# Performance work log

Hardware: AMD Instinct MI355X
Metric: run time of the kernel (lower is better)

Reference implementation:

```python
import jax, jax.numpy as jnp
import numpy as np

H_DIM = 2048
N_HEADS = 16

def setup_inputs() -> dict:
    key = jax.random.key(0)
    ks = jax.random.split(key, 9)
    B, T, C = 2, 2048, H_DIM
    scale = 1.0 / np.sqrt(C)  # lecun_normal approx
    src = jax.random.normal(ks[0], (B, T, C), dtype=jnp.float32)
    Wq = jax.random.normal(ks[1], (C, H_DIM), dtype=jnp.float32) * scale
    Wk = jax.random.normal(ks[2], (C, H_DIM), dtype=jnp.float32) * scale
    Wv = jax.random.normal(ks[3], (C, H_DIM), dtype=jnp.float32) * scale
    Wo = jax.random.normal(ks[4], (H_DIM, H_DIM), dtype=jnp.float32) * scale
    bq = jnp.zeros((H_DIM,), jnp.float32)
    bk = jnp.zeros((H_DIM,), jnp.float32)
    bv = jnp.zeros((H_DIM,), jnp.float32)
    bo = jnp.zeros((H_DIM,), jnp.float32)
    return {"src": src, "Wq": Wq, "bq": bq, "Wk": Wk, "bk": bk,
            "Wv": Wv, "bv": bv, "Wo": Wo, "bo": bo}

def reference(src, Wq, bq, Wk, bk, Wv, bv, Wo, bo):
    B, T, C = src.shape
    N = N_HEADS
    D = C // N
    def heads(x):  # [B,T,h_dim] -> [B,N,T,D]
        return x.reshape(B, T, N, D).transpose(0, 2, 1, 3)
    q = heads(src @ Wq + bq)
    k = heads(src @ Wk + bk)
    v = heads(src @ Wv + bv)
    # scaled dot-product with causal mask
    scores = jnp.einsum('bntd,bnsd->bnts', q, k) / jnp.sqrt(jnp.float32(D))
    causal = jnp.tril(jnp.ones((T, T), dtype=bool))
    scores = jnp.where(causal[None, None], scores, -jnp.inf)
    attn = jax.nn.softmax(scores, axis=-1)
    out = jnp.einsum('bnts,bnsd->bntd', attn, v)  # dropout is identity (drop_p=0)
    out = out.transpose(0, 2, 1, 3).reshape(B, T, N * D)
    return out @ Wo + bo
```

## Files before the change

### kernel.cpp

```cpp
#include <hip/hip_runtime.h>
#include <hip/hip_bf16.h>

typedef float f32x4 __attribute__((ext_vector_type(4)));
typedef __bf16 bf16x8v __attribute__((ext_vector_type(8)));
typedef __bf16 bf16x4v __attribute__((ext_vector_type(4)));
typedef unsigned uint2v __attribute__((ext_vector_type(2)));
typedef bf16x8v __attribute__((may_alias)) bf16x8;
typedef bf16x4v __attribute__((may_alias)) bf16x4;
typedef uint2v __attribute__((may_alias)) u32x2;

typedef __attribute__((address_space(1))) const void gvoid_t;
typedef __attribute__((address_space(3))) void lvoid_t;

#define DEVINL __device__ __forceinline__

#define BDIM 2
#define TDIM 2048
#define CDIM 2048
#define NHEAD 16
#define DHEAD 128
#define MROWS 4096
#define WSZ ((size_t)CDIM * CDIM)
#define XSZ ((size_t)MROWS * CDIM)

#define BARRIER_LGKM() asm volatile("s_waitcnt lgkmcnt(0)\ns_barrier" ::: "memory")

DEVINL __bf16 f2bf(float f) {
  unsigned u = __builtin_bit_cast(unsigned, f);
  u += 0x7fffu + ((u >> 16) & 1u);
  unsigned short h = (unsigned short)(u >> 16);
  return __builtin_bit_cast(__bf16, h);
}

DEVINL unsigned pk2bf_trunc(float lo, float hi) {
  return __builtin_amdgcn_perm(__builtin_bit_cast(unsigned, hi),
                               __builtin_bit_cast(unsigned, lo), 0x07060302);
}

DEVINL void gl2lds16(const void* g, void* l) {
  __builtin_amdgcn_global_load_lds((gvoid_t*)g, (lvoid_t*)l, 16, 0, 0);
}

__global__ void detect_dtype(const unsigned* __restrict__ w,
                             int* __restrict__ flag, int* __restrict__ cnt) {
  const int l = threadIdx.x;
  if (l == 0) *cnt = 0;
  const unsigned word = w[l];
  const unsigned e = (word >> 7) & 0xFFu;
  const int vote = (e >= 0x70u && e <= 0x87u) ? 1 : 0;
  const unsigned long long m = __ballot(vote);
  if (l == 0) *flag = (__popcll(m) >= 32) ? 1 : 0;
}

__global__ __launch_bounds__(256) void cvt_src(const void* __restrict__ in,
                                               __bf16* __restrict__ out,
                                               const int* __restrict__ flag,
                                               int n8) {
  const int i = blockIdx.x * 256 + threadIdx.x;
  if (i >= n8) return;
  if (*flag) {
    ((bf16x8*)out)[i] = ((const bf16x8*)in)[i];
  } else {
    const float* f = (const float*)in + (size_t)i * 8;
    bf16x8v v;
#pragma unroll
    for (int j = 0; j < 8; ++j) v[j] = f2bf(f[j]);
    ((bf16x8*)out)[i] = v;
  }
}

__global__ __launch_bounds__(256) void cvt_wt(
    const void* __restrict__ w0, const void* __restrict__ w1,
    const void* __restrict__ w2, const void* __restrict__ w3,
    __bf16* __restrict__ out, const int* __restrict__ flag) {
  __shared__ __attribute__((aligned(16))) __bf16 tile[64][68];
  const void* W = (blockIdx.z == 0) ? w0 : (blockIdx.z == 1) ? w1
                : (blockIdx.z == 2) ? w2 : w3;
  __bf16* Wt = out + (size_t)blockIdx.z * WSZ;
  const int tx = threadIdx.x & 63, ty = threadIdx.x >> 6;
  const int k0 = blockIdx.x * 64, n0 = blockIdx.y * 64;
  const int fl = *flag;
#pragma unroll
  for (int i = ty; i < 64; i += 4) {
    const size_t off = (size_t)(k0 + i) * CDIM + n0 + tx;
    const float v = fl ? (float)((const __bf16*)W)[off] : ((const float*)W)[off];
    tile[i][tx] = f2bf(v);
  }
  __syncthreads();
#pragma unroll
  for (int i = ty; i < 64; i += 4)
    Wt[(size_t)(n0 + i) * CDIM + k0 + tx] = tile[tx][i];
}

__global__ __launch_bounds__(256) void cvt_bias(
    const void* __restrict__ b0, const void* __restrict__ b1,
    const void* __restrict__ b2, const void* __restrict__ b3,
    float* __restrict__ out, const int* __restrict__ flag) {
  const int i = blockIdx.x * 256 + threadIdx.x;
  const void* b = (i < 2048) ? b0 : (i < 4096) ? b1 : (i < 6144) ? b2 : b3;
  const int idx = i & 2047;
  out[i] = (*flag) ? (float)((const __bf16*)b)[idx] : ((const float*)b)[idx];
}

template <int MODE>
__global__ __launch_bounds__(512, 2) void gemmring(
    const __bf16* __restrict__ A, const __bf16* __restrict__ Bt,
    const float* __restrict__ bias, __bf16* __restrict__ qb,
    __bf16* __restrict__ kb, __bf16* __restrict__ vtb,
    const int* __restrict__ flag, void* __restrict__ outp) {
  constexpr int K = CDIM;
  constexpr int NKT = K / 64;
  __shared__ __attribute__((aligned(16))) __bf16 Asl[4][128 * 32];
  __shared__ __attribute__((aligned(16))) __bf16 Bsl[4][256 * 32];

  const int tid = threadIdx.x;
  const int w = tid >> 6, l = tid & 63;
  const int quad = l >> 4, l16 = l & 15;
  const int wm = w >> 2, wn = w & 3;

  const int bid = blockIdx.x;
  const int bm = bid & 31, bn = bid >> 5;
  const int m0 = bm * 128, n0 = bn * 256;

  const int ls = (tid & 7) ^ ((tid >> 3) & 7);
  const int rbase = 2 * (tid >> 3) + (ls >> 2);
  const int cb8 = (ls & 3) * 8;
  const __bf16* gAh = A + (size_t)(m0 + rbase) * K + cb8;
  const __bf16* gBh = Bt + (size_t)(n0 + rbase) * K + cb8;

  const int L2 = l16 >> 1;
  const int physr = (((l16 & 1) << 2) + quad) ^ L2;
  const int lane_e = L2 * 64 + physr * 8;

#define STAGE_A(h)                                                       \
  gl2lds16(gAh + (size_t)(((h) >> 1) * 64 + ((h) & 1) * 32),             \
           (__bf16*)Asl[(h) & 3] + w * 512)
#define STAGE_B(h, e)                                                    \
  gl2lds16(gBh + (size_t)(e) * 128 * K +                                 \
               (((h) >> 1) * 64 + ((h) & 1) * 32),                       \
           (__bf16*)Bsl[(h) & 3] + (e) * 4096 + w * 512)

  f32x4 acc[4][4];
#pragma unroll
  for (int i = 0; i < 4; ++i)
#pragma unroll
    for (int j = 0; j < 4; ++j) acc[i][j] = (f32x4){0.f, 0.f, 0.f, 0.f};

  STAGE_A(0); STAGE_B(0, 0); STAGE_B(0, 1);
  STAGE_A(1); STAGE_B(1, 0); STAGE_B(1, 1);
  STAGE_A(2); STAGE_B(2, 0); STAGE_B(2, 1);
  asm volatile("s_waitcnt vmcnt(6)" ::: "memory");
  __builtin_amdgcn_sched_barrier(0);
  __builtin_amdgcn_s_barrier();

#define MFMA8(NF0)                                                        \
  __builtin_amdgcn_s_setprio(1);                                          \
  _Pragma("unroll") for (int mi = 0; mi < 4; ++mi) {                      \
    acc[mi][(NF0)] = __builtin_amdgcn_mfma_f32_16x16x32_bf16(             \
        afr[mi], bfr[0], acc[mi][(NF0)], 0, 0, 0);                        \
    acc[mi][(NF0) + 1] = __builtin_amdgcn_mfma_f32_16x16x32_bf16(         \
        afr[mi], bfr[1], acc[mi][(NF0) + 1], 0, 0, 0);                    \
  }                                                                       \
  __builtin_amdgcn_s_setprio(0);

#define LGKM_BAR()                                                        \
  __builtin_amdgcn_s_barrier();                                           \
  asm volatile("s_waitcnt lgkmcnt(0)" ::: "memory");                      \
  __builtin_amdgcn_sched_barrier(0)

  for (int kt = 0; kt < NKT; ++kt) {
    const int h0 = 2 * kt;
    const __bf16* Ab0 = Asl[h0 & 3];
    const __bf16* Bb0 = Bsl[h0 & 3];
    const __bf16* Ab1 = Asl[(h0 + 1) & 3];
    const __bf16* Bb1 = Bsl[(h0 + 1) & 3];
    bf16x8 afr[4], bfr[2];

#pragma unroll
    for (int mi = 0; mi < 4; ++mi)
      afr[mi] = *(const bf16x8*)&Ab0[(wm * 64 + mi * 16) * 32 + lane_e];
    bfr[0] = *(const bf16x8*)&Bb0[(wn * 64 + 0 * 16) * 32 + lane_e];
    bfr[1] = *(const bf16x8*)&Bb0[(wn * 64 + 1 * 16) * 32 + lane_e];
    if (kt <= NKT - 2) { STAGE_A(h0 + 3); STAGE_B(h0 + 3, 0); }
    LGKM_BAR();
    MFMA8(0)
    __builtin_amdgcn_s_barrier();

    bfr[0] = *(const bf16x8*)&Bb0[(wn * 64 + 2 * 16) * 32 + lane_e];
    bfr[1] = *(const bf16x8*)&Bb0[(wn * 64 + 3 * 16) * 32 + lane_e];
    if (kt <= NKT - 2) { STAGE_B(h0 + 3, 1); }
    LGKM_BAR();
    MFMA8(2)
    if (kt < NKT - 1)
      asm volatile("s_waitcnt vmcnt(6)" ::: "memory");
    else
      asm volatile("s_waitcnt vmcnt(0)" ::: "memory");
    __builtin_amdgcn_sched_barrier(0);
    __builtin_amdgcn_s_barrier();

#pragma unroll
    for (int mi = 0; mi < 4; ++mi)
      afr[mi] = *(const bf16x8*)&Ab1[(wm * 64 + mi * 16) * 32 + lane_e];
    bfr[0] = *(const bf16x8*)&Bb1[(wn * 64 + 0 * 16) * 32 + lane_e];
    bfr[1] = *(const bf16x8*)&Bb1[(wn * 64 + 1 * 16) * 32 + lane_e];
    if (kt <= NKT - 3) { STAGE_A(h0 + 4); STAGE_B(h0 + 4, 0); }
    LGKM_BAR();
    MFMA8(0)
    __builtin_amdgcn_s_barrier();

    bfr[0] = *(const bf16x8*)&Bb1[(wn * 64 + 2 * 16) * 32 + lane_e];
    bfr[1] = *(const bf16x8*)&Bb1[(wn * 64 + 3 * 16) * 32 + lane_e];
    if (kt <= NKT - 3) { STAGE_B(h0 + 4, 1); }
    LGKM_BAR();
    MFMA8(2)
    if (kt < NKT - 2)
      asm volatile("s_waitcnt vmcnt(6)" ::: "memory");
    else if (kt == NKT - 2)
      asm volatile("s_waitcnt vmcnt(3)" ::: "memory");
    __builtin_amdgcn_sched_barrier(0);
    __builtin_amdgcn_s_barrier();
  }
#undef MFMA8
#undef LGKM_BAR
#undef STAGE_A
#undef STAGE_B

  if (MODE == 0) {
    const int mat = n0 >> 11;
#pragma unroll
    for (int nf = 0; nf < 4; ++nf) {
      const int n = n0 + wn * 64 + nf * 16 + l16;
      const int nn = n & 2047;
      const int h = nn >> 7, d = nn & 127;
      const float bv = bias[n];
#pragma unroll
      for (int mi = 0; mi < 4; ++mi) {
        const int mbase = m0 + wm * 64 + mi * 16 + quad * 4;
        const int bb = mbase >> 11, t = mbase & 2047;
        if (mat == 2) {
          bf16x4v v4;
#pragma unroll
          for (int r = 0; r < 4; ++r) v4[r] = f2bf(acc[mi][nf][r] + bv);
          *(bf16x4*)&vtb[((size_t)(bb * NHEAD + h) * DHEAD + d) * TDIM + t] = v4;
        } else {
          __bf16* op = (mat == 0) ? qb : kb;
#pragma unroll
          for (int r = 0; r < 4; ++r)
            op[((size_t)(bb * NHEAD + h) * TDIM + t + r) * DHEAD + d] =
                f2bf(acc[mi][nf][r] + bv);
        }
      }
    }
  } else {
    const int ofl = *flag;
#pragma unroll
    for (int nf = 0; nf < 4; ++nf) {
      const int n = n0 + wn * 64 + nf * 16 + l16;
      const float bv = bias[n];
#pragma unroll
      for (int mi = 0; mi < 4; ++mi) {
#pragma unroll
        for (int r = 0; r < 4; ++r) {
          const int m = m0 + wm * 64 + mi * 16 + quad * 4 + r;
          const float v = acc[mi][nf][r] + bv;
          if (ofl) ((__bf16*)outp)[(size_t)m * CDIM + n] = f2bf(v);
          else     ((float*)outp)[(size_t)m * CDIM + n] = v;
        }
      }
    }
  }
}

__global__ __launch_bounds__(256, 2) void attn(
    const __bf16* __restrict__ Q, const __bf16* __restrict__ K,
    const __bf16* __restrict__ Vt, __bf16* __restrict__ ctx,
    int* __restrict__ cnt) {
  constexpr float CSC = 0.12753139726f;
  __shared__ __attribute__((aligned(16))) __bf16 Kls[64 * 128];
  __shared__ __attribute__((aligned(16))) __bf16 Vls[128 * 64];
  __shared__ __attribute__((aligned(16))) __bf16 Pls[4][32 * 64];
  __shared__ int jobLds;

  const int tid = threadIdx.x;
  const int w = tid >> 6, l = tid & 63, quad = l >> 4, l16 = l & 15;

  const int krow = tid >> 4;
  const int kcol = tid & 15;
  const int kldsoff = ((kcol ^ krow) * 8);
  const int vrow = tid >> 3;
  const int vcol = tid & 7;
  const int vldsoff = ((vcol ^ (vrow & 7)) * 8);

  for (;;) {
    __syncthreads();
    if (tid == 0) jobLds = atomicAdd(cnt, 1);
    __syncthreads();
    const int j = jobLds;
    if (j >= 512) break;
    const int qt = 15 - (j >> 5);
    const int bh = j & 31;
    const int t0w = qt * 128 + w * 32;
    const __bf16* Qbh = Q + (size_t)bh * TDIM * DHEAD;
    const __bf16* Kbh = K + (size_t)bh * TDIM * DHEAD;
    const __bf16* Vbh = Vt + (size_t)bh * TDIM * DHEAD;

    bf16x8 qf[2][4];
#pragma unroll
    for (int tt = 0; tt < 2; ++tt)
#pragma unroll
      for (int ks = 0; ks < 4; ++ks)
        qf[tt][ks] = *(const bf16x8*)(Qbh +
                     (size_t)(t0w + tt * 16 + l16) * DHEAD + ks * 32 + quad * 8);

    f32x4 oacc[8][2];
#pragma unroll
    for (int dt = 0; dt < 8; ++dt)
#pragma unroll
      for (int tt = 0; tt < 2; ++tt) oacc[dt][tt] = (f32x4){0.f, 0.f, 0.f, 0.f};
    float mrow[2] = {-1e30f, -1e30f};
    float lrow[2] = {0.f, 0.f};

    const int nsb = 2 * (qt + 1);

    bf16x8 kr[4], vr[4];
#pragma unroll
    for (int p = 0; p < 4; ++p)
      kr[p] = *(const bf16x8*)(Kbh + (size_t)(p * 16 + krow) * DHEAD + kcol * 8);
#pragma unroll
    for (int p = 0; p < 4; ++p)
      vr[p] = *(const bf16x8*)(Vbh + (size_t)(p * 32 + vrow) * TDIM + vcol * 8);

    for (int sb = 0; sb < nsb; ++sb) {
      const int s0 = sb * 64;
      BARRIER_LGKM();
#pragma unroll
      for (int p = 0; p < 4; ++p)
        *(bf16x8*)&Kls[(p * 16 + krow) * 128 + kldsoff] = kr[p];
#pragma unroll
      for (int p = 0; p < 4; ++p)
        *(bf16x8*)&Vls[(p * 32 + vrow) * 64 + vldsoff] = vr[p];
      if (sb + 1 < nsb) {
        const int s1 = s0 + 64;
#pragma unroll
        for (int p = 0; p < 4; ++p)
          kr[p] = *(const bf16x8*)(Kbh + (size_t)(s1 + p * 16 + krow) * DHEAD +
                                   kcol * 8);
#pragma unroll
        for (int p = 0; p < 4; ++p)
          vr[p] = *(const bf16x8*)(Vbh + (size_t)(p * 32 + vrow) * TDIM + s1 +
                                   vcol * 8);
      }
      BARRIER_LGKM();
      if (s0 > t0w + 31) continue;

      f32x4 sacc[4][2];
#pragma unroll
      for (int st = 0; st < 4; ++st)
#pragma unroll
        for (int tt = 0; tt < 2; ++tt) sacc[st][tt] = (f32x4){0.f, 0.f, 0.f, 0.f};
#pragma unroll
      for (int ks = 0; ks < 4; ++ks) {
        bf16x8 kf[4];
#pragma unroll
        for (int st = 0; st < 4; ++st)
          kf[st] = *(const bf16x8*)&Kls[(st * 16 + l16) * 128 +
                                        (((ks * 4 + quad) ^ l16) * 8)];
#pragma unroll
        for (int st = 0; st < 4; ++st)
#pragma unroll
          for (int tt = 0; tt < 2; ++tt)
            sacc[st][tt] = __builtin_amdgcn_mfma_f32_16x16x32_bf16(
                kf[st], qf[tt][ks], sacc[st][tt], 0, 0, 0);
      }
      if (s0 + 63 > t0w) {
#pragma unroll
        for (int st = 0; st < 4; ++st)
#pragma unroll
          for (int tt = 0; tt < 2; ++tt)
#pragma unroll
            for (int r = 0; r < 4; ++r) {
              const int s = s0 + st * 16 + quad * 4 + r;
              const int t = t0w + tt * 16 + l16;
              if (s > t) sacc[st][tt][r] = -1e30f;
            }
      }
#pragma unroll
      for (int tt = 0; tt < 2; ++tt) {
        float vm = -1e30f;
#pragma unroll
        for (int st = 0; st < 4; ++st)
#pragma unroll
          for (int r = 0; r < 4; ++r) vm = fmaxf(vm, sacc[st][tt][r]);
        vm = fmaxf(vm, __shfl_xor(vm, 16));
        vm = fmaxf(vm, __shfl_xor(vm, 32));
        const float mnew = fmaxf(mrow[tt], vm);
        if (__ballot(mnew > mrow[tt])) {
          const float alpha = exp2f((mrow[tt] - mnew) * CSC);
          lrow[tt] *= alpha;
#pragma unroll
          for (int dt = 0; dt < 8; ++dt)
#pragma unroll
            for (int r = 0; r < 4; ++r) oacc[dt][tt][r] *= alpha;
          mrow[tt] = mnew;
        }
        float rs = 0.f;
#pragma unroll
        for (int st = 0; st < 4; ++st) {
          const float p0 = exp2f((sacc[st][tt][0] - mnew) * CSC);
          const float p1 = exp2f((sacc[st][tt][1] - mnew) * CSC);
          const float p2 = exp2f((sacc[st][tt][2] - mnew) * CSC);
          const float p3 = exp2f((sacc[st][tt][3] - mnew) * CSC);
          rs += (p0 + p1) + (p2 + p3);
          u32x2 pk = {pk2bf_trunc(p0, p1), pk2bf_trunc(p2, p3)};
          *(u32x2*)&Pls[w][(tt * 16 + l16) * 64 +
                           (((st * 2 + (quad >> 1)) ^ (l16 & 7)) * 8) +
                           (quad & 1) * 4] = pk;
        }
        rs += __shfl_xor(rs, 16);
        rs += __shfl_xor(rs, 32);
        lrow[tt] += rs;
      }
      asm volatile("s_waitcnt lgkmcnt(0)" ::: "memory");
#pragma unroll
      for (int ks = 0; ks < 2; ++ks) {
        bf16x8 pf[2];
#pragma unroll
        for (int tt = 0; tt < 2; ++tt)
          pf[tt] = *(const bf16x8*)&Pls[w][(tt * 16 + l16) * 64 +
                                           (((ks * 4 + quad) ^ (l16 & 7)) * 8)];
#pragma unroll
        for (int dt = 0; dt < 8; ++dt) {
          const bf16x8 vf =
              *(const bf16x8*)&Vls[(dt * 16 + l16) * 64 +
                                   (((ks * 4 + quad) ^ (l16 & 7)) * 8)];
#pragma unroll
          for (int tt = 0; tt < 2; ++tt)
            oacc[dt][tt] = __builtin_amdgcn_mfma_f32_16x16x32_bf16(
                vf, pf[tt], oacc[dt][tt], 0, 0, 0);
        }
      }
    }

    const int b = bh >> 4, h = bh & 15;
#pragma unroll
    for (int tt = 0; tt < 2; ++tt) {
      const float rinv = 1.0f / lrow[tt];
      const int t = t0w + tt * 16 + l16;
      __bf16* cp = ctx + ((size_t)(b * TDIM + t)) * CDIM + h * DHEAD;
#pragma unroll
      for (int dt = 0; dt < 8; ++dt) {
        bf16x4v v4;
#pragma unroll
        for (int r = 0; r < 4; ++r) v4[r] = f2bf(oacc[dt][tt][r] * rinv);
        *(bf16x4*)&cp[dt * 16 + quad * 4] = v4;
      }
    }
  }
}

extern "C" void kernel_launch(void* const* d_in, const int* in_sizes, int n_in,
                              void* d_out, int out_size, void* d_ws,
                              size_t ws_size, hipStream_t stream) {
  const void* src = d_in[0];
  const void* Wq = d_in[1];
  const void* bq = d_in[2];
  const void* Wk = d_in[3];
  const void* bk = d_in[4];
  const void* Wv = d_in[5];
  const void* bv = d_in[6];
  const void* Wo = d_in[7];
  const void* bo = d_in[8];

  char* wsb = (char*)d_ws;
  int* flag = (int*)wsb;
  int* cnt = (int*)(wsb + 128);
  __bf16* srcbf = (__bf16*)(wsb + 256);
  __bf16* wqt = srcbf + XSZ;
  __bf16* wkt = wqt + WSZ;
  __bf16* wvt = wkt + WSZ;
  __bf16* wot = wvt + WSZ;
  __bf16* qb = wot + WSZ;
  __bf16* kb = qb + XSZ;
  __bf16* vtb = kb + XSZ;
  float* biasf = (float*)(vtb + XSZ);
  __bf16* ctx = srcbf;

  detect_dtype<<<1, 64, 0, stream>>>((const unsigned*)src, flag, cnt);
  cvt_src<<<4096, 256, 0, stream>>>(src, srcbf, flag, (int)(XSZ / 8));
  cvt_wt<<<dim3(32, 32, 4), 256, 0, stream>>>(Wq, Wk, Wv, Wo, wqt, flag);
  cvt_bias<<<32, 256, 0, stream>>>(bq, bk, bv, bo, biasf, flag);
  gemmring<0><<<768, 512, 0, stream>>>(srcbf, wqt, biasf, qb, kb, vtb,
                                       nullptr, nullptr);
  attn<<<512, 256, 0, stream>>>(qb, kb, vtb, ctx, cnt);
  gemmring<1><<<256, 512, 0, stream>>>(ctx, wot, biasf + 6144, nullptr,
                                       nullptr, nullptr, flag, d_out);
}
```

Before: 426.6 us.

## Enlarge GEMM block tiles to 256x256 for QKV and 256x128 for output projection

Rewrites the bf16 GEMM kernel to use 256-row block tiles: the QKV projection uses 256x256 tiles with 128x64 warp tiles, and the output projection uses 256x128 tiles with 64x64 warp tiles. Each warp loads four A fragments and four B fragments and reuses them across 16 MFMAs, which raises arithmetic intensity per LDS read. The prefetch pipeline changes from a three-half-stage lookahead to a two-stage-ahead scheme with new vmcnt thresholds. In exchange, the QKV launch has only 384 blocks, LDS use is larger, and register pressure is higher, which may limit occupancy and leave the 256 CUs unevenly loaded.

```diff
diff --git a/kernel.cpp b/kernel.cpp
--- a/kernel.cpp
+++ b/kernel.cpp
@@ -103,127 +103,161 @@
 }
 
 template <int MODE>
-__global__ __launch_bounds__(512, 2) void gemmring(
+__global__ __launch_bounds__(512, 2) void gemm8p(
     const __bf16* __restrict__ A, const __bf16* __restrict__ Bt,
     const float* __restrict__ bias, __bf16* __restrict__ qb,
     __bf16* __restrict__ kb, __bf16* __restrict__ vtb,
     const int* __restrict__ flag, void* __restrict__ outp) {
   constexpr int K = CDIM;
   constexpr int NKT = K / 64;
-  __shared__ __attribute__((aligned(16))) __bf16 Asl[4][128 * 32];
-  __shared__ __attribute__((aligned(16))) __bf16 Bsl[4][256 * 32];
+  constexpr int BN = (MODE == 0) ? 256 : 128;
+  constexpr int WMR = (MODE == 0) ? 128 : 64;
+  constexpr int MF = WMR / 16;
+  constexpr int BLD = BN / 128;
+  __shared__ __attribute__((aligned(16))) __bf16 Asl[4][256 * 32];
+  __shared__ __attribute__((aligned(16))) __bf16 Bsl[4][BN * 32];
 
   const int tid = threadIdx.x;
   const int w = tid >> 6, l = tid & 63;
   const int quad = l >> 4, l16 = l & 15;
-  const int wm = w >> 2, wn = w & 3;
+  const int wm = (MODE == 0) ? (w >> 2) : (w >> 1);
+  const int wn = (MODE == 0) ? (w & 3) : (w & 1);
 
   const int bid = blockIdx.x;
-  const int bm = bid & 31, bn = bid >> 5;
-  const int m0 = bm * 128, n0 = bn * 256;
+  const int bm = bid & 15, bn = bid >> 4;
+  const int m0 = bm * 256, n0 = bn * BN;
 
   const int ls = (tid & 7) ^ ((tid >> 3) & 7);
   const int rbase = 2 * (tid >> 3) + (ls >> 2);
-  const int cb8 = (ls & 3) * 8;
-  const __bf16* gAh = A + (size_t)(m0 + rbase) * K + cb8;
-  const __bf16* gBh = Bt + (size_t)(n0 + rbase) * K + cb8;
+  const int cb8e = (ls & 3) * 8;
+  const __bf16* gA = A + (size_t)(m0 + rbase) * K + cb8e;
+  const __bf16* gB = Bt + (size_t)(n0 + rbase) * K + cb8e;
 
   const int L2 = l16 >> 1;
-  const int physr = (((l16 & 1) << 2) + quad) ^ L2;
+  const int physr = ((((l16 & 1) << 2) + quad) ^ L2) & 7;
   const int lane_e = L2 * 64 + physr * 8;
-
-#define STAGE_A(h)                                                       \
-  gl2lds16(gAh + (size_t)(((h) >> 1) * 64 + ((h) & 1) * 32),             \
-           (__bf16*)Asl[(h) & 3] + w * 512)
-#define STAGE_B(h, e)                                                    \
-  gl2lds16(gBh + (size_t)(e) * 128 * K +                                 \
-               (((h) >> 1) * 64 + ((h) & 1) * 32),                       \
-           (__bf16*)Bsl[(h) & 3] + (e) * 4096 + w * 512)
-
-  f32x4 acc[4][4];
-#pragma unroll
-  for (int i = 0; i < 4; ++i)
+  const int abase = wm * WMR * 32;
+  const int bbase = wn * 2048;
+
+  f32x4 acc[MF][4];
+#pragma unroll
+  for (int i = 0; i < MF; ++i)
 #pragma unroll
     for (int j = 0; j < 4; ++j) acc[i][j] = (f32x4){0.f, 0.f, 0.f, 0.f};
 
-  STAGE_A(0); STAGE_B(0, 0); STAGE_B(0, 1);
-  STAGE_A(1); STAGE_B(1, 0); STAGE_B(1, 1);
-  STAGE_A(2); STAGE_B(2, 0); STAGE_B(2, 1);
-  asm volatile("s_waitcnt vmcnt(6)" ::: "memory");
-  __builtin_amdgcn_sched_barrier(0);
+#define STAGE_A(h)                                                           \
+  {                                                                          \
+    const int _s = (h) & 3;                                                  \
+    const size_t _c = (size_t)((h) >> 1) * 64 + ((h) & 1) * 32;              \
+    gl2lds16(gA + _c, (__bf16*)Asl[_s] + w * 512);                           \
+    gl2lds16(gA + (size_t)128 * K + _c, (__bf16*)Asl[_s] + 4096 + w * 512);  \
+  }
+#define STAGE_B(h)                                                           \
+  {                                                                          \
+    const int _s = (h) & 3;                                                  \
+    const size_t _c = (size_t)((h) >> 1) * 64 + ((h) & 1) * 32;              \
+    gl2lds16(gB + _c, (__bf16*)Bsl[_s] + w * 512);                           \
+    if (BLD == 2)                                                            \
+      gl2lds16(gB + (size_t)128 * K + _c, (__bf16*)Bsl[_s] + 4096 + w * 512); \
+  }
+#define DS_FRAGS(AP, BP, MI0, DO_B)                                          \
+  _Pragma("unroll") for (int i = 0; i < 4; ++i)                              \
+      afr[i] = *(const bf16x8*)&(AP)[abase + ((MI0) + i) * 512 + lane_e];    \
+  if (DO_B) {                                                                \
+    _Pragma("unroll") for (int nf = 0; nf < 4; ++nf)                         \
+        bfr[nf] = *(const bf16x8*)&(BP)[bbase + nf * 512 + lane_e];          \
+  }
+#define MFMA16(MI0)                                                          \
+  __builtin_amdgcn_s_setprio(1);                                             \
+  _Pragma("unroll") for (int i = 0; i < 4; ++i)                              \
+      _Pragma("unroll") for (int nf = 0; nf < 4; ++nf)                       \
+          acc[(MI0) + i][nf] = __builtin_amdgcn_mfma_f32_16x16x32_bf16(      \
+              afr[i], bfr[nf], acc[(MI0) + i][nf], 0, 0, 0);                 \
+  __builtin_amdgcn_s_setprio(0);
+#define LGKM0()                                                              \
+  asm volatile("s_waitcnt lgkmcnt(0)" ::: "memory");                         \
+  __builtin_amdgcn_sched_barrier(0)
+#define VM_N()                                                               \
+  do {                                                                       \
+    if constexpr (MODE == 0)                                                 \
+      asm volatile("s_waitcnt vmcnt(4)" ::: "memory");                       \
+    else                                                                     \
+      asm volatile("s_waitcnt vmcnt(3)" ::: "memory");                       \
+    __builtin_amdgcn_sched_barrier(0);                                       \
+  } while (0)
+#define VM_0()                                                               \
+  do {                                                                       \
+    asm volatile("s_waitcnt vmcnt(0)" ::: "memory");                         \
+    __builtin_amdgcn_sched_barrier(0);                                       \
+  } while (0)
+
+  STAGE_A(0) STAGE_B(0) STAGE_A(1) STAGE_B(1)
+  VM_N();
   __builtin_amdgcn_s_barrier();
 
-#define MFMA8(NF0)                                                        \
-  __builtin_amdgcn_s_setprio(1);                                          \
-  _Pragma("unroll") for (int mi = 0; mi < 4; ++mi) {                      \
-    acc[mi][(NF0)] = __builtin_amdgcn_mfma_f32_16x16x32_bf16(             \
-        afr[mi], bfr[0], acc[mi][(NF0)], 0, 0, 0);                        \
-    acc[mi][(NF0) + 1] = __builtin_amdgcn_mfma_f32_16x16x32_bf16(         \
-        afr[mi], bfr[1], acc[mi][(NF0) + 1], 0, 0, 0);                    \
-  }                                                                       \
-  __builtin_amdgcn_s_setprio(0);
-
-#define LGKM_BAR()                                                        \
-  __builtin_amdgcn_s_barrier();                                           \
-  asm volatile("s_waitcnt lgkmcnt(0)" ::: "memory");                      \
-  __builtin_amdgcn_sched_barrier(0)
-
   for (int kt = 0; kt < NKT; ++kt) {
-    const int h0 = 2 * kt;
-    const __bf16* Ab0 = Asl[h0 & 3];
-    const __bf16* Bb0 = Bsl[h0 & 3];
-    const __bf16* Ab1 = Asl[(h0 + 1) & 3];
-    const __bf16* Bb1 = Bsl[(h0 + 1) & 3];
-    bf16x8 afr[4], bfr[2];
-
-#pragma unroll
-    for (int mi = 0; mi < 4; ++mi)
-      afr[mi] = *(const bf16x8*)&Ab0[(wm * 64 + mi * 16) * 32 + lane_e];
-    bfr[0] = *(const bf16x8*)&Bb0[(wn * 64 + 0 * 16) * 32 + lane_e];
-    bfr[1] = *(const bf16x8*)&Bb0[(wn * 64 + 1 * 16) * 32 + lane_e];
-    if (kt <= NKT - 2) { STAGE_A(h0 + 3); STAGE_B(h0 + 3, 0); }
-    LGKM_BAR();
-    MFMA8(0)
-    __builtin_amdgcn_s_barrier();
-
-    bfr[0] = *(const bf16x8*)&Bb0[(wn * 64 + 2 * 16) * 32 + lane_e];
-    bfr[1] = *(const bf16x8*)&Bb0[(wn * 64 + 3 * 16) * 32 + lane_e];
-    if (kt <= NKT - 2) { STAGE_B(h0 + 3, 1); }
-    LGKM_BAR();
-    MFMA8(2)
-    if (kt < NKT - 1)
-      asm volatile("s_waitcnt vmcnt(6)" ::: "memory");
-    else
-      asm volatile("s_waitcnt vmcnt(0)" ::: "memory");
-    __builtin_amdgcn_sched_barrier(0);
-    __builtin_amdgcn_s_barrier();
-
-#pragma unroll
-    for (int mi = 0; mi < 4; ++mi)
-      afr[mi] = *(const bf16x8*)&Ab1[(wm * 64 + mi * 16) * 32 + lane_e];
-    bfr[0] = *(const bf16x8*)&Bb1[(wn * 64 + 0 * 16) * 32 + lane_e];
-    bfr[1] = *(const bf16x8*)&Bb1[(wn * 64 + 1 * 16) * 32 + lane_e];
-    if (kt <= NKT - 3) { STAGE_A(h0 + 4); STAGE_B(h0 + 4, 0); }
-    LGKM_BAR();
-    MFMA8(0)
-    __builtin_amdgcn_s_barrier();
-
-    bfr[0] = *(const bf16x8*)&Bb1[(wn * 64 + 2 * 16) * 32 + lane_e];
-    bfr[1] = *(const bf16x8*)&Bb1[(wn * 64 + 3 * 16) * 32 + lane_e];
-    if (kt <= NKT - 3) { STAGE_B(h0 + 4, 1); }
-    LGKM_BAR();
-    MFMA8(2)
-    if (kt < NKT - 2)
-      asm volatile("s_waitcnt vmcnt(6)" ::: "memory");
-    else if (kt == NKT - 2)
-      asm volatile("s_waitcnt vmcnt(3)" ::: "memory");
-    __builtin_amdgcn_sched_barrier(0);
-    __builtin_amdgcn_s_barrier();
-  }
-#undef MFMA8
-#undef LGKM_BAR
+    const __bf16* A0 = Asl[(2 * kt) & 3];
+    const __bf16* B0 = Bsl[(2 * kt) & 3];
+    const __bf16* A1 = Asl[(2 * kt + 1) & 3];
+    const __bf16* B1 = Bsl[(2 * kt + 1) & 3];
+    const bool st = (kt + 1 < NKT);
+    bf16x8 afr[4], bfr[4];
+
+    if (MODE == 0) {
+      DS_FRAGS(A0, B0, 0, 1)
+      if (st) STAGE_A(2 * kt + 2)
+      __builtin_amdgcn_s_barrier();
+      LGKM0();
+      MFMA16(0)
+      __builtin_amdgcn_s_barrier();
+
+      DS_FRAGS(A0, B0, 4, 0)
+      if (st) STAGE_B(2 * kt + 2)
+      __builtin_amdgcn_s_barrier();
+      LGKM0();
+      MFMA16(4)
+      if (st) VM_N(); else VM_0();
+      __builtin_amdgcn_s_barrier();
+
+      DS_FRAGS(A1, B1, 0, 1)
+      if (st) STAGE_A(2 * kt + 3)
+      __builtin_amdgcn_s_barrier();
+      LGKM0();
+      MFMA16(0)
+      __builtin_amdgcn_s_barrier();
+
+      DS_FRAGS(A1, B1, 4, 0)
+      if (st) STAGE_B(2 * kt + 3)
+      __builtin_amdgcn_s_barrier();
+      LGKM0();
+      MFMA16(4)
+      if (st) VM_N();
+      __builtin_amdgcn_s_barrier();
+    } else {
+      DS_FRAGS(A0, B0, 0, 1)
+      if (st) { STAGE_A(2 * kt + 2) STAGE_B(2 * kt + 2) }
+      __builtin_amdgcn_s_barrier();
+      LGKM0();
+      MFMA16(0)
+      if (st) VM_N(); else VM_0();
+      __builtin_amdgcn_s_barrier();
+
+      DS_FRAGS(A1, B1, 0, 1)
+      if (st) { STAGE_A(2 * kt + 3) STAGE_B(2 * kt + 3) }
+      __builtin_amdgcn_s_barrier();
+      LGKM0();
+      MFMA16(0)
+      if (st) VM_N();
+      __builtin_amdgcn_s_barrier();
+    }
+  }
 #undef STAGE_A
 #undef STAGE_B
+#undef DS_FRAGS
+#undef MFMA16
+#undef LGKM0
+#undef VM_N
+#undef VM_0
 
   if (MODE == 0) {
     const int mat = n0 >> 11;
@@ -234,8 +268,8 @@
       const int h = nn >> 7, d = nn & 127;
       const float bv = bias[n];
 #pragma unroll
-      for (int mi = 0; mi < 4; ++mi) {
-        const int mbase = m0 + wm * 64 + mi * 16 + quad * 4;
+      for (int mi = 0; mi < MF; ++mi) {
+        const int mbase = m0 + wm * WMR + mi * 16 + quad * 4;
         const int bb = mbase >> 11, t = mbase & 2047;
         if (mat == 2) {
           bf16x4v v4;
@@ -258,10 +292,10 @@
       const int n = n0 + wn * 64 + nf * 16 + l16;
       const float bv = bias[n];
 #pragma unroll
-      for (int mi = 0; mi < 4; ++mi) {
+      for (int mi = 0; mi < MF; ++mi) {
 #pragma unroll
         for (int r = 0; r < 4; ++r) {
-          const int m = m0 + wm * 64 + mi * 16 + quad * 4 + r;
+          const int m = m0 + wm * WMR + mi * 16 + quad * 4 + r;
           const float v = acc[mi][nf][r] + bv;
           if (ofl) ((__bf16*)outp)[(size_t)m * CDIM + n] = f2bf(v);
           else     ((float*)outp)[(size_t)m * CDIM + n] = v;
@@ -489,9 +523,9 @@
   cvt_src<<<4096, 256, 0, stream>>>(src, srcbf, flag, (int)(XSZ / 8));
   cvt_wt<<<dim3(32, 32, 4), 256, 0, stream>>>(Wq, Wk, Wv, Wo, wqt, flag);
   cvt_bias<<<32, 256, 0, stream>>>(bq, bk, bv, bo, biasf, flag);
-  gemmring<0><<<768, 512, 0, stream>>>(srcbf, wqt, biasf, qb, kb, vtb,
-                                       nullptr, nullptr);
+  gemm8p<0><<<384, 512, 0, stream>>>(srcbf, wqt, biasf, qb, kb, vtb,
+                                     nullptr, nullptr);
   attn<<<512, 256, 0, stream>>>(qb, kb, vtb, ctx, cnt);
-  gemmring<1><<<256, 512, 0, stream>>>(ctx, wot, biasf + 6144, nullptr,
-                                       nullptr, nullptr, flag, d_out);
-}
+  gemm8p<1><<<256, 512, 0, stream>>>(ctx, wot, biasf + 6144, nullptr,
+                                     nullptr, nullptr, flag, d_out);
+}
```

After: 442.7 us. +3.8%, slower.
